# Kernel tuning notes

Hardware: AMD Instinct MI355X
Metric: run time of the kernel (lower is better)

The kernel has to match this reference:

```python
import jax, jax.numpy as jnp
import numpy as np

T, B, E, H, V = 256, 256, 256, 512, 50257
FORGET_BIAS = 1.0  # tf BasicLSTMCell default


def setup_inputs() -> dict:
    key = jax.random.key(0)
    k1, k2, k3, k4 = jax.random.split(key, 4)
    x = jax.random.normal(k1, (T, B, E), dtype=jnp.float32)
    # BasicLSTMCell kernel: [(E+H), 4H], gate order i, j, f, o
    lstm_kernel = jax.random.normal(k2, (E + H, 4 * H), dtype=jnp.float32) * 0.05
    lstm_bias = jnp.zeros((4 * H,), dtype=jnp.float32)
    W_out = jax.random.normal(k3, (H, V), dtype=jnp.float32) * 0.05
    b_out = jax.random.normal(k4, (V,), dtype=jnp.float32) * 0.05
    return {"x": x, "lstm_kernel": lstm_kernel, "lstm_bias": lstm_bias,
            "W_out": W_out, "b_out": b_out}


def reference(x, lstm_kernel, lstm_bias, W_out, b_out):
    # x: [T, B, E] (static_rnn list of timesteps). BasicLSTMCell recurrence.
    h0 = jnp.zeros((x.shape[1], H), dtype=x.dtype)
    c0 = jnp.zeros_like(h0)

    def step(carry, x_t):
        h, c = carry
        gates = jnp.concatenate([x_t, h], axis=-1) @ lstm_kernel + lstm_bias
        i, j, f, o = jnp.split(gates, 4, axis=-1)  # tf gate order: i, j, f, o
        c_new = jax.nn.sigmoid(f + FORGET_BIAS) * c + jax.nn.sigmoid(i) * jnp.tanh(j)
        h_new = jax.nn.sigmoid(o) * jnp.tanh(c_new)
        return (h_new, c_new), None

    (h_last, _), _ = jax.lax.scan(step, (h0, c0), x)
    # Final dense projection on last output only
    return h_last @ W_out + b_out  # [B, V]
```

## Files before the change

### kernel.cpp

```cpp
#include <hip/hip_runtime.h>
#include <hip/hip_bf16.h>

#define T_DIM 256
#define B_DIM 256
#define E_DIM 256
#define H_DIM 512
#define V_DIM 50257
#define BH    (B_DIM * H_DIM)
#define PRE_AHEAD 5
#define SENT  0x7F7F7F7Fu

typedef __attribute__((ext_vector_type(8))) short short8;
typedef __attribute__((ext_vector_type(4))) float f32x4;
typedef __attribute__((ext_vector_type(4))) unsigned int uint4v;
typedef __attribute__((ext_vector_type(2))) unsigned int uint2v;

#define MFMA __builtin_amdgcn_mfma_f32_16x16x32_bf16

__device__ __forceinline__ unsigned short f2bf(float f) {
    union { float f; unsigned u; } v; v.f = f;
    unsigned r = v.u + 0x7FFFu + ((v.u >> 16) & 1u);
    return (unsigned short)(r >> 16);
}
__device__ __forceinline__ short cvt_bf(float f) { return (short)f2bf(f); }
__device__ __forceinline__ float sigmoidf_(float x) {
    return 1.0f / (1.0f + __expf(-x));
}
__device__ __forceinline__ float tanhf_(float x) {
    float xc = fminf(fmaxf(x, -15.0f), 15.0f);
    float e = __expf(2.0f * xc);
    return (e - 1.0f) / (e + 1.0f);
}

__device__ __forceinline__ short8 load16_cached(const unsigned short* p) {
    short8 r;
    asm volatile("global_load_dwordx4 %0, %1, off"
                 : "=v"(r) : "v"(p) : "memory");
    return r;
}
__device__ __forceinline__ short8 load16_mall(const unsigned short* p) {
    short8 r;
    asm volatile("global_load_dwordx4 %0, %1, off sc0 sc1"
                 : "=v"(r) : "v"(p) : "memory");
    return r;
}
__device__ __forceinline__ void store8_mall(unsigned short* p, uint2v v) {
    asm volatile("global_store_dwordx2 %0, %1, off sc0 sc1"
                 :: "v"(p), "v"(v) : "memory");
}
__device__ __forceinline__ bool frag_ready(short8 v) {
    union { short8 s; uint4v u; } c; c.s = v;
    return (c.u[0] != SENT) & (c.u[1] != SENT) & (c.u[2] != SENT) & (c.u[3] != SENT);
}

__global__ void __launch_bounds__(128, 1)
lstm_persist(const float* __restrict__ x,
             const float* __restrict__ wk,
             const float* __restrict__ bias,
             unsigned short* __restrict__ hbuf)
{
    extern __shared__ unsigned short lds_w[];
    const int tid = threadIdx.x;
    const int blk = blockIdx.x;
    const int bg  = blk & 7;
    const int hg  = blk >> 3;
    const int bb  = bg * 32;
    const int hh  = hg * 16;

    for (int f = 0; f < 96; ++f) {
        const int kt = f >> 2, g = f & 3;
        for (int idx = tid; idx < 512; idx += 128) {
            const int c  = idx & 15;
            const int hi = (idx >> 4) & 3;
            const int j  = idx >> 6;
            const int k  = kt * 32 + hi * 8 + j;
            const int col = g * 512 + hh + c;
            lds_w[(f * 64 + hi * 16 + c) * 8 + j] = f2bf(wk[(size_t)k * 2048 + col]);
        }
    }
    __syncthreads();

    const int w    = tid >> 6;
    const int lane = tid & 63;
    const int lc   = lane & 15;
    const int lk   = lane >> 4;

    const f32x4 bi  = *(const f32x4*)(bias + 0 * 512 + hh + lk * 4);
    const f32x4 bj  = *(const f32x4*)(bias + 1 * 512 + hh + lk * 4);
    f32x4       bf_ = *(const f32x4*)(bias + 2 * 512 + hh + lk * 4);
    const f32x4 bo  = *(const f32x4*)(bias + 3 * 512 + hh + lk * 4);
    bf_ = bf_ + 1.0f;

    f32x4 c_frag = {0.f, 0.f, 0.f, 0.f};

    const int arow = bb + w * 16 + lc;
    const float* xrow = x + (size_t)arow * E_DIM + lk * 8;
    const size_t hrow_off = (size_t)arow * H_DIM + lk * 8;
    const size_t hsto_off = (size_t)arow * H_DIM + hh + lk * 4;

    f32x4 xreg[16];
    #pragma unroll
    for (int k = 0; k < 8; ++k) {
        xreg[2 * k]     = *(const f32x4*)(xrow + k * 32);
        xreg[2 * k + 1] = *(const f32x4*)(xrow + k * 32 + 4);
    }

    const uint2v sentv = {SENT, SENT};

    for (int t = 0; t < T_DIM; ++t) {
        f32x4 a0 = {0.f,0.f,0.f,0.f}, a1 = a0, a2 = a0, a3 = a0;
        short8 apk[8];
        #pragma unroll
        for (int kt = 0; kt < 8; ++kt) {
            const f32x4 lo = xreg[2 * kt];
            const f32x4 hi = xreg[2 * kt + 1];
            short8 a;
            a[0]=cvt_bf(lo[0]); a[1]=cvt_bf(lo[1]); a[2]=cvt_bf(lo[2]); a[3]=cvt_bf(lo[3]);
            a[4]=cvt_bf(hi[0]); a[5]=cvt_bf(hi[1]); a[6]=cvt_bf(hi[2]); a[7]=cvt_bf(hi[3]);
            apk[kt] = a;
        }
        #pragma unroll
        for (int kt = 0; kt < 8; ++kt) {
            const unsigned short* wp = lds_w + ((size_t)(kt * 4) * 64 + lane) * 8;
            a0 = MFMA(*(const short8*)(wp +    0), apk[kt], a0, 0,0,0);
            a1 = MFMA(*(const short8*)(wp +  512), apk[kt], a1, 0,0,0);
            a2 = MFMA(*(const short8*)(wp + 1024), apk[kt], a2, 0,0,0);
            a3 = MFMA(*(const short8*)(wp + 1536), apk[kt], a3, 0,0,0);
        }

        if (t > 0) {
            const unsigned short* hr = hbuf + (size_t)t * BH + hrow_off;
            short8 hfr[16];
            #pragma unroll
            for (int k = 0; k < 16; ++k)
                hfr[k] = load16_cached(hr + k * 32);
            asm volatile("s_waitcnt vmcnt(0)" ::: "memory");
            __builtin_amdgcn_sched_barrier(0);

            unsigned pend = 0;
            #pragma unroll
            for (int k = 0; k < 16; ++k)
                pend |= frag_ready(hfr[k]) ? 0u : (1u << k);
            #pragma unroll 1
            while (!__all(pend == 0)) {
                #pragma unroll
                for (int k = 0; k < 16; ++k)
                    if (pend & (1u << k)) hfr[k] = load16_mall(hr + k * 32);
                asm volatile("s_waitcnt vmcnt(0)" ::: "memory");
                __builtin_amdgcn_sched_barrier(0);
                unsigned np = 0;
                #pragma unroll
                for (int k = 0; k < 16; ++k)
                    if (pend & (1u << k))
                        np |= frag_ready(hfr[k]) ? 0u : (1u << k);
                pend = np;
            }
            __builtin_amdgcn_sched_barrier(0);

            if (t + 1 < T_DIM) {
                const float* xn = xrow + (size_t)(t + 1) * (B_DIM * E_DIM);
                #pragma unroll
                for (int k = 0; k < 8; ++k) {
                    xreg[2 * k]     = *(const f32x4*)(xn + k * 32);
                    xreg[2 * k + 1] = *(const f32x4*)(xn + k * 32 + 4);
                }
            }

            #pragma unroll
            for (int k = 0; k < 16; ++k) {
                const unsigned short* wp = lds_w + ((size_t)((8 + k) * 4) * 64 + lane) * 8;
                a0 = MFMA(*(const short8*)(wp +    0), hfr[k], a0, 0,0,0);
                a1 = MFMA(*(const short8*)(wp +  512), hfr[k], a1, 0,0,0);
                a2 = MFMA(*(const short8*)(wp + 1024), hfr[k], a2, 0,0,0);
                a3 = MFMA(*(const short8*)(wp + 1536), hfr[k], a3, 0,0,0);
            }
        } else {
            const float* xn = xrow + (size_t)(B_DIM * E_DIM);
            #pragma unroll
            for (int k = 0; k < 8; ++k) {
                xreg[2 * k]     = *(const f32x4*)(xn + k * 32);
                xreg[2 * k + 1] = *(const f32x4*)(xn + k * 32 + 4);
            }
        }

        unsigned short hu[4];
        #pragma unroll
        for (int j = 0; j < 4; ++j) {
            const float iv = a0[j] + bi[j];
            const float jv = a1[j] + bj[j];
            const float fv = a2[j] + bf_[j];
            const float ov = a3[j] + bo[j];
            const float cn = sigmoidf_(fv) * c_frag[j] + sigmoidf_(iv) * tanhf_(jv);
            c_frag[j] = cn;
            hu[j] = f2bf(sigmoidf_(ov) * tanhf_(cn));
        }
        uint2v pk;
        pk[0] = (unsigned)hu[0] | ((unsigned)hu[1] << 16);
        pk[1] = (unsigned)hu[2] | ((unsigned)hu[3] << 16);
        store8_mall(hbuf + (size_t)(t + 1) * BH + hsto_off, pk);
        if (t + PRE_AHEAD <= T_DIM) {
            store8_mall(hbuf + (size_t)(t + PRE_AHEAD) * BH + hsto_off, sentv);
        }
    }
}

__global__ void __launch_bounds__(256)
proj_gemm(const unsigned short* __restrict__ h,
          const float* __restrict__ wout,
          const float* __restrict__ bout,
          float* __restrict__ out)
{
    const int tid  = threadIdx.x;
    const int w    = tid >> 6;
    const int lane = tid & 63;
    const int lc   = lane & 15;
    const int lk   = lane >> 4;
    const int n0   = blockIdx.x * 128 + w * 32;

    f32x4 acc[16][2];
    #pragma unroll
    for (int mt = 0; mt < 16; ++mt) {
        acc[mt][0] = (f32x4){0.f,0.f,0.f,0.f};
        acc[mt][1] = (f32x4){0.f,0.f,0.f,0.f};
    }
    int ncl[2];
    ncl[0] = min(n0 + lc,      V_DIM - 1);
    ncl[1] = min(n0 + 16 + lc, V_DIM - 1);

    #pragma unroll 4
    for (int kt = 0; kt < 16; ++kt) {
        short8 bfr[2];
        #pragma unroll
        for (int nt = 0; nt < 2; ++nt) {
            #pragma unroll
            for (int j = 0; j < 8; ++j) {
                const int k = kt * 32 + lk * 8 + j;
                bfr[nt][j] = (short)f2bf(wout[(size_t)k * V_DIM + ncl[nt]]);
            }
        }
        #pragma unroll
        for (int mt = 0; mt < 16; ++mt) {
            const short8 a = *(const short8*)(h + (size_t)(mt * 16 + lc) * H_DIM
                                                + kt * 32 + lk * 8);
            acc[mt][0] = MFMA(a, bfr[0], acc[mt][0], 0,0,0);
            acc[mt][1] = MFMA(a, bfr[1], acc[mt][1], 0,0,0);
        }
    }

    #pragma unroll
    for (int nt = 0; nt < 2; ++nt) {
        const int n = n0 + nt * 16 + lc;
        if (n < V_DIM) {
            const float bb = bout[n];
            #pragma unroll
            for (int mt = 0; mt < 16; ++mt)
                #pragma unroll
                for (int j = 0; j < 4; ++j)
                    out[(size_t)(mt * 16 + lk * 4 + j) * V_DIM + n] = acc[mt][nt][j] + bb;
        }
    }
}

extern "C" void kernel_launch(void* const* d_in, const int* in_sizes, int n_in,
                              void* d_out, int out_size, void* d_ws, size_t ws_size,
                              hipStream_t stream) {
    const float* x    = (const float*)d_in[0];
    const float* wk   = (const float*)d_in[1];
    const float* bias = (const float*)d_in[2];
    const float* wout = (const float*)d_in[3];
    const float* bout = (const float*)d_in[4];
    float* out = (float*)d_out;

    unsigned short* hbuf = (unsigned short*)d_ws;

    hipMemsetAsync(hbuf, 0x7F, (size_t)PRE_AHEAD * BH * 2, stream);

    hipFuncSetAttribute((const void*)lstm_persist,
                        hipFuncAttributeMaxDynamicSharedMemorySize, 96 * 1024);

    hipLaunchKernelGGL(lstm_persist, dim3(256), dim3(128), 96 * 1024, stream,
                       x, wk, bias, hbuf);
    hipLaunchKernelGGL(proj_gemm, dim3((V_DIM + 127) / 128), dim3(256), 0, stream,
                       hbuf + (size_t)T_DIM * BH, wout, bout, out);
}
```

Baseline: 1.277 ms.

## Precompute input-gate projections for all timesteps before the recurrent loop

Adds a first phase inside the persistent LSTM kernel that computes x_t·W_x for every timestep up front and stores the results as fp16 in a workspace buffer. The recurrent loop then only loads these precomputed gate contributions, prefetched one step ahead, which removes the x MFMAs and x loads from the serial critical path. It also switches the initial h fragment loads from inline asm to plain loads. The cost is a large extra workspace (about 64MB), the extra memory traffic to write and read it, and a reduction of input-gate precision to fp16. A fallback kernel with the old schedule is used when the workspace is too small.

After: 2.028 ms. 58.8% more time.

```diff
diff --git a/kernel.cpp b/kernel.cpp
--- a/kernel.cpp
+++ b/kernel.cpp
@@ -32,12 +32,28 @@
     return (e - 1.0f) / (e + 1.0f);
 }
 
-__device__ __forceinline__ short8 load16_cached(const unsigned short* p) {
+__device__ __forceinline__ short8 pack_h8(f32x4 x, f32x4 y) {
     short8 r;
-    asm volatile("global_load_dwordx4 %0, %1, off"
-                 : "=v"(r) : "v"(p) : "memory");
+    #pragma unroll
+    for (int i = 0; i < 4; ++i) {
+        _Float16 a = (_Float16)x[i];
+        _Float16 b = (_Float16)y[i];
+        r[i]     = *reinterpret_cast<short*>(&a);
+        r[4 + i] = *reinterpret_cast<short*>(&b);
+    }
     return r;
 }
+__device__ __forceinline__ f32x4 unpack_h4(short8 v, int off) {
+    f32x4 r;
+    #pragma unroll
+    for (int i = 0; i < 4; ++i) {
+        short s = v[off + i];
+        _Float16 h = *reinterpret_cast<_Float16*>(&s);
+        r[i] = (float)h;
+    }
+    return r;
+}
+
 __device__ __forceinline__ short8 load16_mall(const unsigned short* p) {
     short8 r;
     asm volatile("global_load_dwordx4 %0, %1, off sc0 sc1"
@@ -52,21 +68,33 @@
     union { short8 s; uint4v u; } c; c.s = v;
     return (c.u[0] != SENT) & (c.u[1] != SENT) & (c.u[2] != SENT) & (c.u[3] != SENT);
 }
-
-__global__ void __launch_bounds__(128, 1)
-lstm_persist(const float* __restrict__ x,
-             const float* __restrict__ wk,
-             const float* __restrict__ bias,
-             unsigned short* __restrict__ hbuf)
+__device__ __forceinline__ void sweep_converge(short8 (&hfr)[16],
+                                               const unsigned short* hr)
 {
-    extern __shared__ unsigned short lds_w[];
-    const int tid = threadIdx.x;
-    const int blk = blockIdx.x;
-    const int bg  = blk & 7;
-    const int hg  = blk >> 3;
-    const int bb  = bg * 32;
-    const int hh  = hg * 16;
-
+    unsigned pend = 0;
+    #pragma unroll
+    for (int k = 0; k < 16; ++k)
+        pend |= frag_ready(hfr[k]) ? 0u : (1u << k);
+    #pragma unroll 1
+    while (!__all(pend == 0)) {
+        #pragma unroll
+        for (int k = 0; k < 16; ++k)
+            if (pend & (1u << k)) hfr[k] = load16_mall(hr + k * 32);
+        asm volatile("s_waitcnt vmcnt(0)" ::: "memory");
+        __builtin_amdgcn_sched_barrier(0);
+        unsigned np = 0;
+        #pragma unroll
+        for (int k = 0; k < 16; ++k)
+            if (pend & (1u << k))
+                np |= frag_ready(hfr[k]) ? 0u : (1u << k);
+        pend = np;
+    }
+    __builtin_amdgcn_sched_barrier(0);
+}
+
+__device__ __forceinline__ void preload_w(unsigned short* lds_w,
+                                          const float* wk, int hh, int tid)
+{
     for (int f = 0; f < 96; ++f) {
         const int kt = f >> 2, g = f & 3;
         for (int idx = tid; idx < 512; idx += 128) {
@@ -78,12 +106,79 @@
             lds_w[(f * 64 + hi * 16 + c) * 8 + j] = f2bf(wk[(size_t)k * 2048 + col]);
         }
     }
+}
+
+__global__ void __launch_bounds__(128, 1)
+lstm_persist_gx(const float* __restrict__ x,
+                const float* __restrict__ wk,
+                const float* __restrict__ bias,
+                unsigned short* __restrict__ hbuf,
+                unsigned short* __restrict__ gx)
+{
+    extern __shared__ unsigned short lds_w[];
+    const int tid = threadIdx.x;
+    const int blk = blockIdx.x;
+    const int bg  = blk & 7;
+    const int hg  = blk >> 3;
+    const int bb  = bg * 32;
+    const int hh  = hg * 16;
+
+    preload_w(lds_w, wk, hh, tid);
     __syncthreads();
 
     const int w    = tid >> 6;
     const int lane = tid & 63;
     const int lc   = lane & 15;
     const int lk   = lane >> 4;
+
+    const int arow = bb + w * 16 + lc;
+    const float* xrow = x + (size_t)arow * E_DIM + lk * 8;
+    const size_t hrow_off = (size_t)arow * H_DIM + lk * 8;
+    const size_t hsto_off = (size_t)arow * H_DIM + hh + lk * 4;
+
+    #define GXP(t) (gx + ((((size_t)(t)) * 256 + blk) * 128 + tid) * 16)
+
+    {
+        f32x4 xreg[16];
+        #pragma unroll
+        for (int k = 0; k < 8; ++k) {
+            xreg[2*k]   = *(const f32x4*)(xrow + k * 32);
+            xreg[2*k+1] = *(const f32x4*)(xrow + k * 32 + 4);
+        }
+        for (int t = 0; t < T_DIM; ++t) {
+            short8 apk[8];
+            #pragma unroll
+            for (int kt = 0; kt < 8; ++kt) {
+                const f32x4 lo = xreg[2*kt], hi = xreg[2*kt+1];
+                short8 a;
+                a[0]=cvt_bf(lo[0]); a[1]=cvt_bf(lo[1]); a[2]=cvt_bf(lo[2]); a[3]=cvt_bf(lo[3]);
+                a[4]=cvt_bf(hi[0]); a[5]=cvt_bf(hi[1]); a[6]=cvt_bf(hi[2]); a[7]=cvt_bf(hi[3]);
+                apk[kt] = a;
+            }
+            if (t + 1 < T_DIM) {
+                const float* xn = xrow + (size_t)(t + 1) * (B_DIM * E_DIM);
+                #pragma unroll
+                for (int k = 0; k < 8; ++k) {
+                    xreg[2*k]   = *(const f32x4*)(xn + k * 32);
+                    xreg[2*k+1] = *(const f32x4*)(xn + k * 32 + 4);
+                }
+            }
+            f32x4 a0 = {0.f,0.f,0.f,0.f}, a1 = a0, a2 = a0, a3 = a0;
+            #pragma unroll
+            for (int kt = 0; kt < 8; ++kt) {
+                const unsigned short* wp = lds_w + ((size_t)(kt * 4) * 64 + lane) * 8;
+                a0 = MFMA(*(const short8*)(wp +    0), apk[kt], a0, 0,0,0);
+                a1 = MFMA(*(const short8*)(wp +  512), apk[kt], a1, 0,0,0);
+                a2 = MFMA(*(const short8*)(wp + 1024), apk[kt], a2, 0,0,0);
+                a3 = MFMA(*(const short8*)(wp + 1536), apk[kt], a3, 0,0,0);
+            }
+            unsigned short* gp = (unsigned short*)GXP(t);
+            *(short8*)(gp)     = pack_h8(a0, a1);
+            *(short8*)(gp + 8) = pack_h8(a2, a3);
+        }
+        asm volatile("s_waitcnt vmcnt(0)" ::: "memory");
+        __builtin_amdgcn_sched_barrier(0);
+    }
 
     const f32x4 bi  = *(const f32x4*)(bias + 0 * 512 + hh + lk * 4);
     const f32x4 bj  = *(const f32x4*)(bias + 1 * 512 + hh + lk * 4);
@@ -92,79 +187,28 @@
     bf_ = bf_ + 1.0f;
 
     f32x4 c_frag = {0.f, 0.f, 0.f, 0.f};
-
-    const int arow = bb + w * 16 + lc;
-    const float* xrow = x + (size_t)arow * E_DIM + lk * 8;
-    const size_t hrow_off = (size_t)arow * H_DIM + lk * 8;
-    const size_t hsto_off = (size_t)arow * H_DIM + hh + lk * 4;
-
-    f32x4 xreg[16];
-    #pragma unroll
-    for (int k = 0; k < 8; ++k) {
-        xreg[2 * k]     = *(const f32x4*)(xrow + k * 32);
-        xreg[2 * k + 1] = *(const f32x4*)(xrow + k * 32 + 4);
-    }
-
     const uint2v sentv = {SENT, SENT};
 
+    short8 gxc0 = *(const short8*)GXP(0);
+    short8 gxc1 = *(const short8*)(GXP(0) + 8);
+
     for (int t = 0; t < T_DIM; ++t) {
-        f32x4 a0 = {0.f,0.f,0.f,0.f}, a1 = a0, a2 = a0, a3 = a0;
-        short8 apk[8];
-        #pragma unroll
-        for (int kt = 0; kt < 8; ++kt) {
-            const f32x4 lo = xreg[2 * kt];
-            const f32x4 hi = xreg[2 * kt + 1];
-            short8 a;
-            a[0]=cvt_bf(lo[0]); a[1]=cvt_bf(lo[1]); a[2]=cvt_bf(lo[2]); a[3]=cvt_bf(lo[3]);
-            a[4]=cvt_bf(hi[0]); a[5]=cvt_bf(hi[1]); a[6]=cvt_bf(hi[2]); a[7]=cvt_bf(hi[3]);
-            apk[kt] = a;
-        }
-        #pragma unroll
-        for (int kt = 0; kt < 8; ++kt) {
-            const unsigned short* wp = lds_w + ((size_t)(kt * 4) * 64 + lane) * 8;
-            a0 = MFMA(*(const short8*)(wp +    0), apk[kt], a0, 0,0,0);
-            a1 = MFMA(*(const short8*)(wp +  512), apk[kt], a1, 0,0,0);
-            a2 = MFMA(*(const short8*)(wp + 1024), apk[kt], a2, 0,0,0);
-            a3 = MFMA(*(const short8*)(wp + 1536), apk[kt], a3, 0,0,0);
-        }
+        f32x4 a0 = unpack_h4(gxc0, 0);
+        f32x4 a1 = unpack_h4(gxc0, 4);
+        f32x4 a2 = unpack_h4(gxc1, 0);
+        f32x4 a3 = unpack_h4(gxc1, 4);
+
+        const int tn = (t + 1 < T_DIM) ? t + 1 : t;
+        short8 gxn0 = *(const short8*)GXP(tn);
+        short8 gxn1 = *(const short8*)(GXP(tn) + 8);
 
         if (t > 0) {
             const unsigned short* hr = hbuf + (size_t)t * BH + hrow_off;
             short8 hfr[16];
             #pragma unroll
             for (int k = 0; k < 16; ++k)
-                hfr[k] = load16_cached(hr + k * 32);
-            asm volatile("s_waitcnt vmcnt(0)" ::: "memory");
-            __builtin_amdgcn_sched_barrier(0);
-
-            unsigned pend = 0;
-            #pragma unroll
-            for (int k = 0; k < 16; ++k)
-                pend |= frag_ready(hfr[k]) ? 0u : (1u << k);
-            #pragma unroll 1
-            while (!__all(pend == 0)) {
-                #pragma unroll
-                for (int k = 0; k < 16; ++k)
-                    if (pend & (1u << k)) hfr[k] = load16_mall(hr + k * 32);
-                asm volatile("s_waitcnt vmcnt(0)" ::: "memory");
-                __builtin_amdgcn_sched_barrier(0);
-                unsigned np = 0;
-                #pragma unroll
-                for (int k = 0; k < 16; ++k)
-                    if (pend & (1u << k))
-                        np |= frag_ready(hfr[k]) ? 0u : (1u << k);
-                pend = np;
-            }
-            __builtin_amdgcn_sched_barrier(0);
-
-            if (t + 1 < T_DIM) {
-                const float* xn = xrow + (size_t)(t + 1) * (B_DIM * E_DIM);
-                #pragma unroll
-                for (int k = 0; k < 8; ++k) {
-                    xreg[2 * k]     = *(const f32x4*)(xn + k * 32);
-                    xreg[2 * k + 1] = *(const f32x4*)(xn + k * 32 + 4);
-                }
-            }
+                hfr[k] = *(const short8*)(hr + k * 32);
+            sweep_converge(hfr, hr);
 
             #pragma unroll
             for (int k = 0; k < 16; ++k) {
@@ -173,13 +217,6 @@
                 a1 = MFMA(*(const short8*)(wp +  512), hfr[k], a1, 0,0,0);
                 a2 = MFMA(*(const short8*)(wp + 1024), hfr[k], a2, 0,0,0);
                 a3 = MFMA(*(const short8*)(wp + 1536), hfr[k], a3, 0,0,0);
-            }
-        } else {
-            const float* xn = xrow + (size_t)(B_DIM * E_DIM);
-            #pragma unroll
-            for (int k = 0; k < 8; ++k) {
-                xreg[2 * k]     = *(const f32x4*)(xn + k * 32);
-                xreg[2 * k + 1] = *(const f32x4*)(xn + k * 32 + 4);
             }
         }
 
@@ -198,9 +235,124 @@
         pk[0] = (unsigned)hu[0] | ((unsigned)hu[1] << 16);
         pk[1] = (unsigned)hu[2] | ((unsigned)hu[3] << 16);
         store8_mall(hbuf + (size_t)(t + 1) * BH + hsto_off, pk);
-        if (t + PRE_AHEAD <= T_DIM) {
+        if (t + PRE_AHEAD <= T_DIM)
             store8_mall(hbuf + (size_t)(t + PRE_AHEAD) * BH + hsto_off, sentv);
-        }
+
+        gxc0 = gxn0;
+        gxc1 = gxn1;
+    }
+    #undef GXP
+}
+
+__global__ void __launch_bounds__(128, 1)
+lstm_persist_fb(const float* __restrict__ x,
+                const float* __restrict__ wk,
+                const float* __restrict__ bias,
+                unsigned short* __restrict__ hbuf)
+{
+    extern __shared__ unsigned short lds_w[];
+    const int tid = threadIdx.x;
+    const int blk = blockIdx.x;
+    const int bg  = blk & 7;
+    const int hg  = blk >> 3;
+    const int bb  = bg * 32;
+    const int hh  = hg * 16;
+
+    preload_w(lds_w, wk, hh, tid);
+    __syncthreads();
+
+    const int w    = tid >> 6;
+    const int lane = tid & 63;
+    const int lc   = lane & 15;
+    const int lk   = lane >> 4;
+
+    const f32x4 bi  = *(const f32x4*)(bias + 0 * 512 + hh + lk * 4);
+    const f32x4 bj  = *(const f32x4*)(bias + 1 * 512 + hh + lk * 4);
+    f32x4       bf_ = *(const f32x4*)(bias + 2 * 512 + hh + lk * 4);
+    const f32x4 bo  = *(const f32x4*)(bias + 3 * 512 + hh + lk * 4);
+    bf_ = bf_ + 1.0f;
+
+    f32x4 c_frag = {0.f, 0.f, 0.f, 0.f};
+    const int arow = bb + w * 16 + lc;
+    const float* xrow = x + (size_t)arow * E_DIM + lk * 8;
+    const size_t hrow_off = (size_t)arow * H_DIM + lk * 8;
+    const size_t hsto_off = (size_t)arow * H_DIM + hh + lk * 4;
+
+    f32x4 xreg[16];
+    #pragma unroll
+    for (int k = 0; k < 8; ++k) {
+        xreg[2*k]   = *(const f32x4*)(xrow + k * 32);
+        xreg[2*k+1] = *(const f32x4*)(xrow + k * 32 + 4);
+    }
+    const uint2v sentv = {SENT, SENT};
+
+    for (int t = 0; t < T_DIM; ++t) {
+        f32x4 a0 = {0.f,0.f,0.f,0.f}, a1 = a0, a2 = a0, a3 = a0;
+        short8 apk[8];
+        #pragma unroll
+        for (int kt = 0; kt < 8; ++kt) {
+            const f32x4 lo = xreg[2*kt], hi = xreg[2*kt+1];
+            short8 a;
+            a[0]=cvt_bf(lo[0]); a[1]=cvt_bf(lo[1]); a[2]=cvt_bf(lo[2]); a[3]=cvt_bf(lo[3]);
+            a[4]=cvt_bf(hi[0]); a[5]=cvt_bf(hi[1]); a[6]=cvt_bf(hi[2]); a[7]=cvt_bf(hi[3]);
+            apk[kt] = a;
+        }
+        #pragma unroll
+        for (int kt = 0; kt < 8; ++kt) {
+            const unsigned short* wp = lds_w + ((size_t)(kt * 4) * 64 + lane) * 8;
+            a0 = MFMA(*(const short8*)(wp +    0), apk[kt], a0, 0,0,0);
+            a1 = MFMA(*(const short8*)(wp +  512), apk[kt], a1, 0,0,0);
+            a2 = MFMA(*(const short8*)(wp + 1024), apk[kt], a2, 0,0,0);
+            a3 = MFMA(*(const short8*)(wp + 1536), apk[kt], a3, 0,0,0);
+        }
+        if (t > 0) {
+            const unsigned short* hr = hbuf + (size_t)t * BH + hrow_off;
+            short8 hfr[16];
+            #pragma unroll
+            for (int k = 0; k < 16; ++k)
+                hfr[k] = *(const short8*)(hr + k * 32);
+            sweep_converge(hfr, hr);
+            if (t + 1 < T_DIM) {
+                const float* xn = xrow + (size_t)(t + 1) * (B_DIM * E_DIM);
+                #pragma unroll
+                for (int k = 0; k < 8; ++k) {
+                    xreg[2*k]   = *(const f32x4*)(xn + k * 32);
+                    xreg[2*k+1] = *(const f32x4*)(xn + k * 32 + 4);
+                }
+            }
+            #pragma unroll
+            for (int k = 0; k < 16; ++k) {
+                const unsigned short* wp = lds_w + ((size_t)((8 + k) * 4) * 64 + lane) * 8;
+                a0 = MFMA(*(const short8*)(wp +    0), hfr[k], a0, 0,0,0);
+                a1 = MFMA(*(const short8*)(wp +  512), hfr[k], a1, 0,0,0);
+                a2 = MFMA(*(const short8*)(wp + 1024), hfr[k], a2, 0,0,0);
+                a3 = MFMA(*(const short8*)(wp + 1536), hfr[k], a3, 0,0,0);
+            }
+        } else {
+            const float* xn = xrow + (size_t)(B_DIM * E_DIM);
+            #pragma unroll
+            for (int k = 0; k < 8; ++k) {
+                xreg[2*k]   = *(const f32x4*)(xn + k * 32);
+                xreg[2*k+1] = *(const f32x4*)(xn + k * 32 + 4);
+            }
+        }
+        unsigned short hu[4];
+        #pragma unroll
+        for (int j = 0; j < 4; ++j) {
+            const float iv = a0[j] + bi[j];
+            const float jv = a1[j] + bj[j];
+            const float fv = a2[j] + bf_[j];
+            const float ov = a3[j] + bo[j];
+            const float cn = sigmoidf_(fv) * c_frag[j] + sigmoidf_(iv) * tanhf_(jv);
+            c_frag[j] = cn;
+            hu[j] = f2bf(sigmoidf_(ov) * tanhf_(cn));
+        }
+        uint2v pk;
+        pk[0] = (unsigned)hu[0] | ((unsigned)hu[1] << 16);
+        pk[1] = (unsigned)hu[2] | ((unsigned)hu[3] << 16);
+        store8_mall(hbuf + (size_t)(t + 1) * BH + hsto_off, pk);
+        if (t + PRE_AHEAD <= T_DIM)
+            store8_mall(hbuf + (size_t)(t + PRE_AHEAD) * BH + hsto_off, sentv);
     }
 }
 
@@ -271,15 +423,27 @@
     const float* bout = (const float*)d_in[4];
     float* out = (float*)d_out;
 
-    unsigned short* hbuf = (unsigned short*)d_ws;
-
-    hipMemsetAsync(hbuf, 0x7F, (size_t)PRE_AHEAD * BH * 2, stream);
-
-    hipFuncSetAttribute((const void*)lstm_persist,
-                        hipFuncAttributeMaxDynamicSharedMemorySize, 96 * 1024);
-
-    hipLaunchKernelGGL(lstm_persist, dim3(256), dim3(128), 96 * 1024, stream,
-                       x, wk, bias, hbuf);
-    hipLaunchKernelGGL(proj_gemm, dim3((V_DIM + 127) / 128), dim3(256), 0, stream,
-                       hbuf + (size_t)T_DIM * BH, wout, bout, out);
-}
+    const size_t GXB = (size_t)T_DIM * B_DIM * 4 * H_DIM * 2;
+    const size_t HBB = (size_t)(T_DIM + 1) * BH * 2;
+
+    if (ws_size >= GXB + HBB) {
+        unsigned short* gxb  = (unsigned short*)d_ws;
+        unsigned short* hbuf = (unsigned short*)((char*)d_ws + GXB);
+        hipMemsetAsync(hbuf, 0x7F, (size_t)PRE_AHEAD * BH * 2, stream);
+        hipFuncSetAttribute((const void*)lstm_persist_gx,
+                            hipFuncAttributeMaxDynamicSharedMemorySize, 96 * 1024);
+        hipLaunchKernelGGL(lstm_persist_gx, dim3(256), dim3(128), 96 * 1024, stream,
+                           x, wk, bias, hbuf, gxb);
+        hipLaunchKernelGGL(proj_gemm, dim3((V_DIM + 127) / 128), dim3(256), 0, stream,
+                           hbuf + (size_t)T_DIM * BH, wout, bout, out);
+    } else {
+        unsigned short* hbuf = (unsigned short*)d_ws;
+        hipMemsetAsync(hbuf, 0x7F, (size_t)PRE_AHEAD * BH * 2, stream);
+        hipFuncSetAttribute((const void*)lstm_persist_fb,
+                            hipFuncAttributeMaxDynamicSharedMemorySize, 96 * 1024);
+        hipLaunchKernelGGL(lstm_persist_fb, dim3(256), dim3(128), 96 * 1024, stream,
+                           x, wk, bias, hbuf);
+        hipLaunchKernelGGL(proj_gemm, dim3((V_DIM + 127) / 128), dim3(256), 0, stream,
+                           hbuf + (size_t)T_DIM * BH, wout, bout, out);
+    }
+}
```

## Overlap h-fragment MFMAs with spin-polling by consuming ready fragments early

Applied to the files above, without the earlier changes.

The persistent LSTM kernel spin-waits on per-fragment sentinels for the previous step's hidden state. Instead of waiting until all 16 fragments are ready before any recurrent MFMA, it now issues MFMAs for fragments as soon as they become ready and re-polls only the missing ones. The first load changes from inline asm to a plain C++ load, which lets the compiler schedule it. This hides some polling latency behind matrix work, at the cost of more code size and branches. The plain load may also change caching or ordering behaviour for the sentinel check.

New measurement: 1.718 ms. 1.35x slower.

```diff
diff --git a/kernel.cpp b/kernel.cpp
--- a/kernel.cpp
+++ b/kernel.cpp
@@ -32,12 +32,6 @@
     return (e - 1.0f) / (e + 1.0f);
 }
 
-__device__ __forceinline__ short8 load16_cached(const unsigned short* p) {
-    short8 r;
-    asm volatile("global_load_dwordx4 %0, %1, off"
-                 : "=v"(r) : "v"(p) : "memory");
-    return r;
-}
 __device__ __forceinline__ short8 load16_mall(const unsigned short* p) {
     short8 r;
     asm volatile("global_load_dwordx4 %0, %1, off sc0 sc1"
@@ -133,7 +127,7 @@
             short8 hfr[16];
             #pragma unroll
             for (int k = 0; k < 16; ++k)
-                hfr[k] = load16_cached(hr + k * 32);
+                hfr[k] = *(const short8*)(hr + k * 32);
             asm volatile("s_waitcnt vmcnt(0)" ::: "memory");
             __builtin_amdgcn_sched_barrier(0);
 
@@ -141,39 +135,69 @@
             #pragma unroll
             for (int k = 0; k < 16; ++k)
                 pend |= frag_ready(hfr[k]) ? 0u : (1u << k);
-            #pragma unroll 1
-            while (!__all(pend == 0)) {
+            unsigned wpend = 0;
+            #pragma unroll
+            for (int k = 0; k < 16; ++k)
+                if (!__all((pend & (1u << k)) == 0)) wpend |= 1u << k;
+
+            #define HMFMA(k)                                                              \
+                {                                                                         \
+                    const unsigned short* wp =                                            \
+                        lds_w + ((size_t)((8 + (k)) * 4) * 64 + lane) * 8;                \
+                    a0 = MFMA(*(const short8*)(wp +    0), hfr[k], a0, 0,0,0);            \
+                    a1 = MFMA(*(const short8*)(wp +  512), hfr[k], a1, 0,0,0);            \
+                    a2 = MFMA(*(const short8*)(wp + 1024), hfr[k], a2, 0,0,0);            \
+                    a3 = MFMA(*(const short8*)(wp + 1536), hfr[k], a3, 0,0,0);            \
+                }
+
+            if (wpend == 0) {
+                if (t + 1 < T_DIM) {
+                    const float* xn = xrow + (size_t)(t + 1) * (B_DIM * E_DIM);
+                    #pragma unroll
+                    for (int k = 0; k < 8; ++k) {
+                        xreg[2 * k]     = *(const f32x4*)(xn + k * 32);
+                        xreg[2 * k + 1] = *(const f32x4*)(xn + k * 32 + 4);
+                    }
+                }
                 #pragma unroll
                 for (int k = 0; k < 16; ++k)
-                    if (pend & (1u << k)) hfr[k] = load16_mall(hr + k * 32);
-                asm volatile("s_waitcnt vmcnt(0)" ::: "memory");
-                __builtin_amdgcn_sched_barrier(0);
-                unsigned np = 0;
+                    HMFMA(k);
+            } else {
                 #pragma unroll
                 for (int k = 0; k < 16; ++k)
-                    if (pend & (1u << k))
-                        np |= frag_ready(hfr[k]) ? 0u : (1u << k);
-                pend = np;
-            }
-            __builtin_amdgcn_sched_barrier(0);
-
-            if (t + 1 < T_DIM) {
-                const float* xn = xrow + (size_t)(t + 1) * (B_DIM * E_DIM);
+                    if (wpend & (1u << k)) hfr[k] = load16_mall(hr + k * 32);
                 #pragma unroll
-                for (int k = 0; k < 8; ++k) {
-                    xreg[2 * k]     = *(const f32x4*)(xn + k * 32);
-                    xreg[2 * k + 1] = *(const f32x4*)(xn + k * 32 + 4);
+                for (int k = 0; k < 16; ++k)
+                    if (!(wpend & (1u << k))) HMFMA(k);
+                #pragma unroll 1
+                while (wpend) {
+                    asm volatile("s_waitcnt vmcnt(0)" ::: "memory");
+                    __builtin_amdgcn_sched_barrier(0);
+                    unsigned newly = 0;
+                    #pragma unroll
+                    for (int k = 0; k < 16; ++k)
+                        if ((wpend & (1u << k)) && __all(frag_ready(hfr[k])))
+                            newly |= 1u << k;
+                    const unsigned rem = wpend & ~newly;
+                    #pragma unroll
+                    for (int k = 0; k < 16; ++k)
+                        if (rem & (1u << k)) hfr[k] = load16_mall(hr + k * 32);
+                    #pragma unroll
+                    for (int k = 0; k < 16; ++k)
+                        if (newly & (1u << k)) HMFMA(k);
+                    wpend = rem;
+                }
+                __builtin_amdgcn_sched_barrier(0);
+                if (t + 1 < T_DIM) {
+                    const float* xn = xrow + (size_t)(t + 1) * (B_DIM * E_DIM);
+                    #pragma unroll
+                    for (int k = 0; k < 8; ++k) {
+                        xreg[2 * k]     = *(const f32x4*)(xn + k * 32);
+                        xreg[2 * k + 1] = *(const f32x4*)(xn + k * 32 + 4);
+                    }
                 }
             }
-
-            #pragma unroll
-            for (int k = 0; k < 16; ++k) {
-                const unsigned short* wp = lds_w + ((size_t)((8 + k) * 4) * 64 + lane) * 8;
-                a0 = MFMA(*(const short8*)(wp +    0), hfr[k], a0, 0,0,0);
-                a1 = MFMA(*(const short8*)(wp +  512), hfr[k], a1, 0,0,0);
-                a2 = MFMA(*(const short8*)(wp + 1024), hfr[k], a2, 0,0,0);
-                a3 = MFMA(*(const short8*)(wp + 1536), hfr[k], a3, 0,0,0);
-            }
+            #undef HMFMA
         } else {
             const float* xn = xrow + (size_t)(B_DIM * E_DIM);
             #pragma unroll
```
